# Kernel tuning notes

Measured on AMD Instinct MI355X. Metric: run time of the kernel, lower is better.

## Reference

```python
import jax, jax.numpy as jnp
import numpy as np
import math

B, N, E, H = 2, 4096, 256, 8
HS = E // H  # head_size = 32


def setup_inputs() -> dict:
    key = jax.random.key(0)
    ks = jax.random.split(key, 8)
    s = 1.0 / math.sqrt(E)
    return {
        "node_features": jax.random.normal(ks[0], (B, N, E), dtype=jnp.float32),
        "adj": jax.random.randint(ks[1], (B, N, N), 0, 2).astype(jnp.bool_),
        "Wq": jax.random.normal(ks[2], (E, E), dtype=jnp.float32) * s,
        "bq": jax.random.normal(ks[3], (E,), dtype=jnp.float32) * s,
        "Wk": jax.random.normal(ks[4], (E, E), dtype=jnp.float32) * s,
        "bk": jax.random.normal(ks[5], (E,), dtype=jnp.float32) * s,
        "Wv": jax.random.normal(ks[6], (E, E), dtype=jnp.float32) * s,
        "bv": jax.random.normal(ks[7], (E,), dtype=jnp.float32) * s,
    }


def _split_heads(x):
    # (B, N, E) -> (B, H, N, HS)
    return x.reshape(B, N, H, HS).transpose(0, 2, 1, 3)


def reference(node_features, adj, Wq, bq, Wk, bk, Wv, bv):
    # nn.Linear: x @ W.T + b
    Q = _split_heads(node_features @ Wq.T + bq)
    K = _split_heads(node_features @ Wk.T + bk)
    V = _split_heads(node_features @ Wv.T + bv)
    scores = jnp.einsum("bhnd,bhmd->bhnm", Q, K) / math.sqrt(HS)
    scores = jnp.where(adj[:, None, :, :], scores, -jnp.inf)
    probs = jax.nn.softmax(scores, axis=-1)
    out = jnp.einsum("bhnm,bhmd->bhnd", probs, V)
    # (B, H, N, HS) -> (B, N, E); note: original forward does NOT apply W_out
    return out.transpose(0, 2, 1, 3).reshape(B, N, E)
```

## Files before the change

### kernel.cpp

```cpp
#include <hip/hip_runtime.h>

typedef __attribute__((ext_vector_type(8))) short short8;
typedef __attribute__((ext_vector_type(4))) float f32x4;
typedef __attribute__((ext_vector_type(4))) unsigned short u16x4;

constexpr int cB = 2, cN = 4096, cE = 256, cH = 8, cHS = 32;

__device__ __forceinline__ unsigned short f2bf(float f) {
    unsigned int u = __builtin_bit_cast(unsigned int, f);
    u = (u + 0x7FFFu + ((u >> 16) & 1u)) >> 16;
    return (unsigned short)u;
}

__device__ __forceinline__ unsigned int cvt_pk_bf16(float lo, float hi) {
    unsigned int r;
    asm("v_cvt_pk_bf16_f32 %0, %1, %2" : "=v"(r) : "v"(lo), "v"(hi));
    return r;
}

__global__ __launch_bounds__(256) void cvt_x_kernel(const float* __restrict__ x,
                                                    unsigned short* __restrict__ xb) {
    int t = blockIdx.x * 256 + threadIdx.x;
    f32x4 v = *((const f32x4*)x + t);
    u16x4 o = { f2bf(v[0]), f2bf(v[1]), f2bf(v[2]), f2bf(v[3]) };
    *((u16x4*)xb + t) = o;
}

__global__ __launch_bounds__(256) void cvt_w_kernel(const float* __restrict__ Wq,
                                                    const float* __restrict__ Wk,
                                                    const float* __restrict__ Wv,
                                                    unsigned short* __restrict__ wcb) {
    int t = blockIdx.x * 256 + threadIdx.x;
    int f = t * 4;
    int o = f >> 8, i = f & 255;
    const float* src = (o < 256) ? Wq : (o < 512 ? Wk : Wv);
    f32x4 v = *(const f32x4*)(src + (size_t)(o & 255) * 256 + i);
    u16x4 ov = { f2bf(v[0]), f2bf(v[1]), f2bf(v[2]), f2bf(v[3]) };
    *((u16x4*)wcb + t) = ov;
}

__global__ __launch_bounds__(256) void bitpack_kernel(const int* __restrict__ adj,
                                                      unsigned long long* __restrict__ mask) {
    int lane = threadIdx.x & 63;
    int wave = blockIdx.x * 4 + (threadIdx.x >> 6);
    const int nwaves = 2048 * 4;
    const int nwords = cB * cN * cN / 64;
    for (int w = wave; w < nwords; w += nwaves) {
        int v = adj[(size_t)w * 64 + lane];
        unsigned long long bal = __ballot(v != 0);
        if (lane == 0) mask[w] = bal;
    }
}

__global__ __launch_bounds__(256) void qkv_proj_kernel(const unsigned short* __restrict__ xb,
                                                       const unsigned short* __restrict__ wcb,
                                                       const float* __restrict__ bq,
                                                       const float* __restrict__ bk,
                                                       const float* __restrict__ bv,
                                                       unsigned short* __restrict__ Qb,
                                                       unsigned short* __restrict__ Kb,
                                                       unsigned short* __restrict__ Vt) {
    const int wv = threadIdx.x >> 6, lane = threadIdx.x & 63;
    const int col = lane & 15, grp = lane >> 4;
    const int rowbase = blockIdx.x * 64 + wv * 16;
    const int colbase = blockIdx.y * 64;
    const float CE = 1.4426950408889634f * 0.17677669529663687f;
    f32x4 acc[4] = {};
    for (int kk = 0; kk < 8; ++kk) {
        short8 a = *(const short8*)(xb + (size_t)(rowbase + col) * 256 + kk * 32 + grp * 8);
        #pragma unroll
        for (int c = 0; c < 4; ++c) {
            short8 bf = *(const short8*)(wcb + (size_t)(colbase + c * 16 + col) * 256 + kk * 32 + grp * 8);
            acc[c] = __builtin_amdgcn_mfma_f32_16x16x32_bf16(a, bf, acc[c], 0, 0, 0);
        }
    }
    #pragma unroll
    for (int c = 0; c < 4; ++c) {
        const int o = colbase + c * 16 + col;
        const int sel = o >> 8, oo = o & 255;
        const float bias = (sel == 0 ? bq : sel == 1 ? bk : bv)[oo];
        const int h = oo >> 5, hs = oo & 31;
        const int R0 = rowbase + grp * 4;
        const int b = R0 >> 12, n0 = R0 & 4095;
        if (sel == 0) {
            #pragma unroll
            for (int r = 0; r < 4; ++r)
                Qb[(size_t)((b * cH + h) * cN + n0 + r) * cHS + hs] = f2bf((acc[c][r] + bias) * CE);
        } else if (sel == 1) {
            #pragma unroll
            for (int r = 0; r < 4; ++r)
                Kb[(size_t)((b * cH + h) * cN + n0 + r) * cHS + hs] = f2bf(acc[c][r] + bias);
        } else {
            unsigned short* vrow = Vt + (size_t)((b * cH + h) * cHS + hs) * cN;
            #pragma unroll
            for (int r = 0; r < 4; ++r) {
                const int n = n0 + r;
                const int pos = (n & ~31) + 2 * (n & 15) + ((n >> 4) & 1);
                vrow[pos] = f2bf(acc[c][r] + bias);
            }
        }
    }
}

__global__ __launch_bounds__(256, 4) void attn_kernel(const unsigned short* __restrict__ Qb,
                                                      const unsigned short* __restrict__ Kb,
                                                      const unsigned short* __restrict__ Vt,
                                                      const unsigned int* __restrict__ mask32,
                                                      float* __restrict__ out) {
    __shared__ float comb[4][64][24];
    const int wv = threadIdx.x >> 6, lane = threadIdx.x & 63;
    const int col = lane & 15, grp = lane >> 4;
    int bid = blockIdx.x;
    bid = (bid & 7) * 128 + (bid >> 3);
    const int qt0 = bid & 63, h = (bid >> 6) & 7, b = bid >> 9;
    const unsigned short* Qh = Qb + (size_t)(b * cH + h) * cN * cHS;
    const unsigned short* Kh = Kb + (size_t)(b * cH + h) * cN * cHS;
    const unsigned short* Vh = Vt + (size_t)(b * cH + h) * cHS * cN;
    unsigned int* pw = (unsigned int*)&comb[0][0][0] + wv * 640;
    const f32x4 z4 = {0.f, 0.f, 0.f, 0.f};
    const short8 ones = { 0x3F80, 0x3F80, 0x3F80, 0x3F80, 0x3F80, 0x3F80, 0x3F80, 0x3F80 };
    const int kt0 = wv * 32;

    #pragma unroll 1
    for (int tk = 0; tk < 2; ++tk) {
        const int qbase = (qt0 + tk * 64) * 32;
        const unsigned int* mrow = mask32 + (size_t)(b * cN + qbase) * 128;

        const short8 aq0 = *(const short8*)(Qh + (size_t)(qbase + col) * cHS + grp * 8);
        const short8 aq1 = *(const short8*)(Qh + (size_t)(qbase + 16 + col) * cHS + grp * 8);

        f32x4 acc[2][2] = {};
        f32x4 lacc[2] = {};

        short8 ck0 = *(const short8*)(Kh + (size_t)(kt0 * 32 + col) * cHS + grp * 8);
        short8 ck1 = *(const short8*)(Kh + (size_t)(kt0 * 32 + 16 + col) * cHS + grp * 8);
        short8 cv0 = *(const short8*)(Vh + (size_t)col * cN + kt0 * 32 + grp * 8);
        short8 cv1 = *(const short8*)(Vh + (size_t)(16 + col) * cN + kt0 * 32 + grp * 8);
        unsigned int cm[8];
        #pragma unroll
        for (int i = 0; i < 8; ++i)
            cm[i] = mrow[(size_t)((i >> 2) * 16 + grp * 4 + (i & 3)) * 128 + kt0];

        #pragma unroll 2
        for (int kt = kt0; kt < kt0 + 32; ++kt) {
            const short8 k0 = ck0, k1 = ck1, v0 = cv0, v1 = cv1;
            unsigned int m8[8];
            #pragma unroll
            for (int i = 0; i < 8; ++i) m8[i] = cm[i];
            if (kt < kt0 + 31) {
                const int kb = (kt + 1) * 32;
                ck0 = *(const short8*)(Kh + (size_t)(kb + col) * cHS + grp * 8);
                ck1 = *(const short8*)(Kh + (size_t)(kb + 16 + col) * cHS + grp * 8);
                cv0 = *(const short8*)(Vh + (size_t)col * cN + kb + grp * 8);
                cv1 = *(const short8*)(Vh + (size_t)(16 + col) * cN + kb + grp * 8);
                #pragma unroll
                for (int i = 0; i < 8; ++i)
                    cm[i] = mrow[(size_t)((i >> 2) * 16 + grp * 4 + (i & 3)) * 128 + kt + 1];
            }

            f32x4 s[2][2];
            s[0][0] = __builtin_amdgcn_mfma_f32_16x16x32_bf16(aq0, k0, z4, 0, 0, 0);
            s[0][1] = __builtin_amdgcn_mfma_f32_16x16x32_bf16(aq0, k1, z4, 0, 0, 0);
            s[1][0] = __builtin_amdgcn_mfma_f32_16x16x32_bf16(aq1, k0, z4, 0, 0, 0);
            s[1][1] = __builtin_amdgcn_mfma_f32_16x16x32_bf16(aq1, k1, z4, 0, 0, 0);

            #pragma unroll
            for (int qs = 0; qs < 2; ++qs) {
                #pragma unroll
                for (int r = 0; r < 4; ++r) {
                    const unsigned int w32 = m8[qs * 4 + r];
                    const float e0 = __builtin_exp2f(s[qs][0][r]);
                    const float e1 = __builtin_exp2f(s[qs][1][r]);
                    const unsigned int msk = ((w32 >> col) & 0x00010001u) * 0xFFFFu;
                    pw[qs * 320 + (grp * 4 + r) * 20 + col] = cvt_pk_bf16(e0, e1) & msk;
                }
            }
            #pragma unroll
            for (int qs = 0; qs < 2; ++qs) {
                const short8 pa = *(const short8*)(pw + qs * 320 + col * 20 + grp * 4);
                acc[qs][0] = __builtin_amdgcn_mfma_f32_16x16x32_bf16(pa, v0, acc[qs][0], 0, 0, 0);
                acc[qs][1] = __builtin_amdgcn_mfma_f32_16x16x32_bf16(pa, v1, acc[qs][1], 0, 0, 0);
                lacc[qs]   = __builtin_amdgcn_mfma_f32_16x16x32_bf16(pa, ones, lacc[qs], 0, 0, 0);
            }
        }

        __syncthreads();
        float* me = &comb[wv][lane][0];
        *(f32x4*)(me +  0) = acc[0][0];
        *(f32x4*)(me +  4) = acc[0][1];
        *(f32x4*)(me +  8) = acc[1][0];
        *(f32x4*)(me + 12) = acc[1][1];
        *(f32x4*)(me + 16) = lacc[0];
        *(f32x4*)(me + 20) = lacc[1];
        __syncthreads();

        const int sg = wv, qs2 = sg >> 1, half = sg & 1;
        f32x4 a = {0.f, 0.f, 0.f, 0.f};
        f32x4 l = {0.f, 0.f, 0.f, 0.f};
        #pragma unroll
        for (int w = 0; w < 4; ++w) {
            a += *(const f32x4*)&comb[w][lane][sg * 4];
            l += *(const f32x4*)&comb[w][lane][16 + qs2 * 4];
        }
        const int row0 = qbase + qs2 * 16 + grp * 4;
        #pragma unroll
        for (int j = 0; j < 4; ++j) {
            out[(size_t)(b * cN + row0 + j) * cE + h * 32 + half * 16 + col] = a[j] / l[j];
        }
        __syncthreads();
    }
}

extern "C" void kernel_launch(void* const* d_in, const int* in_sizes, int n_in,
                              void* d_out, int out_size, void* d_ws, size_t ws_size,
                              hipStream_t stream) {
    const float* x   = (const float*)d_in[0];
    const int*   adj = (const int*)d_in[1];
    const float* Wq  = (const float*)d_in[2];
    const float* bq  = (const float*)d_in[3];
    const float* Wk  = (const float*)d_in[4];
    const float* bk  = (const float*)d_in[5];
    const float* Wv  = (const float*)d_in[6];
    const float* bv  = (const float*)d_in[7];
    float* out = (float*)d_out;

    char* ws = (char*)d_ws;
    unsigned short* Xb  = (unsigned short*)(ws);
    unsigned short* Wcb = (unsigned short*)(ws + (4ull << 20));
    unsigned short* Qb  = (unsigned short*)(ws + (5ull << 20));
    unsigned short* Kb  = (unsigned short*)(ws + (9ull << 20));
    unsigned short* Vt  = (unsigned short*)(ws + (13ull << 20));
    unsigned long long* mask64 = (unsigned long long*)(ws + (17ull << 20));

    cvt_x_kernel<<<dim3(2048), dim3(256), 0, stream>>>(x, Xb);
    cvt_w_kernel<<<dim3(192), dim3(256), 0, stream>>>(Wq, Wk, Wv, Wcb);
    bitpack_kernel<<<dim3(2048), dim3(256), 0, stream>>>(adj, mask64);
    qkv_proj_kernel<<<dim3(128, 12), dim3(256), 0, stream>>>(Xb, Wcb, bq, bk, bv, Qb, Kb, Vt);
    attn_kernel<<<dim3(1024), dim3(256), 0, stream>>>(Qb, Kb, Vt, (const unsigned int*)mask64, out);
}
```

Before: 212.5 us.

## Software-pipeline attention loop: overlap PV MFMA of previous tile with current scores

Restructures the per-wave key loop into a skewed software pipeline. A prologue computes probabilities for the first tile, and each iteration then issues the P·V MFMAs for the previous tile before computing exp/mask/pack for the current tile. An epilogue drains the last tile. Mask words are now loaded in the same iteration they are used, while K is prefetched one tile ahead and V is loaded for the tile it is consumed in one iteration later. The goal is to hide MFMA latency behind exp work. The trade-offs are unroll 1 instead of 2 and less prefetch distance for the mask and V loads.

```diff
diff --git a/kernel.cpp b/kernel.cpp
--- a/kernel.cpp
+++ b/kernel.cpp
@@ -132,31 +132,42 @@
         f32x4 acc[2][2] = {};
         f32x4 lacc[2] = {};
 
-        short8 ck0 = *(const short8*)(Kh + (size_t)(kt0 * 32 + col) * cHS + grp * 8);
-        short8 ck1 = *(const short8*)(Kh + (size_t)(kt0 * 32 + 16 + col) * cHS + grp * 8);
-        short8 cv0 = *(const short8*)(Vh + (size_t)col * cN + kt0 * 32 + grp * 8);
-        short8 cv1 = *(const short8*)(Vh + (size_t)(16 + col) * cN + kt0 * 32 + grp * 8);
-        unsigned int cm[8];
-        #pragma unroll
-        for (int i = 0; i < 8; ++i)
-            cm[i] = mrow[(size_t)((i >> 2) * 16 + grp * 4 + (i & 3)) * 128 + kt0];
-
-        #pragma unroll 2
-        for (int kt = kt0; kt < kt0 + 32; ++kt) {
-            const short8 k0 = ck0, k1 = ck1, v0 = cv0, v1 = cv1;
+        short8 kc0 = *(const short8*)(Kh + (size_t)(kt0 * 32 + col) * cHS + grp * 8);
+        short8 kc1 = *(const short8*)(Kh + (size_t)(kt0 * 32 + 16 + col) * cHS + grp * 8);
+        short8 vp0 = *(const short8*)(Vh + (size_t)col * cN + kt0 * 32 + grp * 8);
+        short8 vp1 = *(const short8*)(Vh + (size_t)(16 + col) * cN + kt0 * 32 + grp * 8);
+        {
+            f32x4 s[2][2];
+            s[0][0] = __builtin_amdgcn_mfma_f32_16x16x32_bf16(aq0, kc0, z4, 0, 0, 0);
+            s[0][1] = __builtin_amdgcn_mfma_f32_16x16x32_bf16(aq0, kc1, z4, 0, 0, 0);
+            s[1][0] = __builtin_amdgcn_mfma_f32_16x16x32_bf16(aq1, kc0, z4, 0, 0, 0);
+            s[1][1] = __builtin_amdgcn_mfma_f32_16x16x32_bf16(aq1, kc1, z4, 0, 0, 0);
+            #pragma unroll
+            for (int qs = 0; qs < 2; ++qs)
+                #pragma unroll
+                for (int r = 0; r < 4; ++r) {
+                    const unsigned int w32 = mrow[(size_t)(qs * 16 + grp * 4 + r) * 128 + kt0];
+                    const float e0 = __builtin_exp2f(s[qs][0][r]);
+                    const float e1 = __builtin_exp2f(s[qs][1][r]);
+                    const unsigned int msk = ((w32 >> col) & 0x00010001u) * 0xFFFFu;
+                    pw[qs * 320 + (grp * 4 + r) * 20 + col] = cvt_pk_bf16(e0, e1) & msk;
+                }
+        }
+        short8 kn0 = *(const short8*)(Kh + (size_t)((kt0 + 1) * 32 + col) * cHS + grp * 8);
+        short8 kn1 = *(const short8*)(Kh + (size_t)((kt0 + 1) * 32 + 16 + col) * cHS + grp * 8);
+
+        #pragma unroll 1
+        for (int kt = kt0 + 1; kt < kt0 + 32; ++kt) {
+            const short8 k0 = kn0, k1 = kn1;
+            const int kb1 = (kt + 1) * 32;
+            kn0 = *(const short8*)(Kh + (size_t)(kb1 + col) * cHS + grp * 8);
+            kn1 = *(const short8*)(Kh + (size_t)(kb1 + 16 + col) * cHS + grp * 8);
+            const short8 vc0 = *(const short8*)(Vh + (size_t)col * cN + kt * 32 + grp * 8);
+            const short8 vc1 = *(const short8*)(Vh + (size_t)(16 + col) * cN + kt * 32 + grp * 8);
             unsigned int m8[8];
             #pragma unroll
-            for (int i = 0; i < 8; ++i) m8[i] = cm[i];
-            if (kt < kt0 + 31) {
-                const int kb = (kt + 1) * 32;
-                ck0 = *(const short8*)(Kh + (size_t)(kb + col) * cHS + grp * 8);
-                ck1 = *(const short8*)(Kh + (size_t)(kb + 16 + col) * cHS + grp * 8);
-                cv0 = *(const short8*)(Vh + (size_t)col * cN + kb + grp * 8);
-                cv1 = *(const short8*)(Vh + (size_t)(16 + col) * cN + kb + grp * 8);
-                #pragma unroll
-                for (int i = 0; i < 8; ++i)
-                    cm[i] = mrow[(size_t)((i >> 2) * 16 + grp * 4 + (i & 3)) * 128 + kt + 1];
-            }
+            for (int i = 0; i < 8; ++i)
+                m8[i] = mrow[(size_t)((i >> 2) * 16 + grp * 4 + (i & 3)) * 128 + kt];
 
             f32x4 s[2][2];
             s[0][0] = __builtin_amdgcn_mfma_f32_16x16x32_bf16(aq0, k0, z4, 0, 0, 0);
@@ -166,6 +177,14 @@
 
             #pragma unroll
             for (int qs = 0; qs < 2; ++qs) {
+                const short8 pa = *(const short8*)(pw + qs * 320 + col * 20 + grp * 4);
+                acc[qs][0] = __builtin_amdgcn_mfma_f32_16x16x32_bf16(pa, vp0, acc[qs][0], 0, 0, 0);
+                acc[qs][1] = __builtin_amdgcn_mfma_f32_16x16x32_bf16(pa, vp1, acc[qs][1], 0, 0, 0);
+                lacc[qs]   = __builtin_amdgcn_mfma_f32_16x16x32_bf16(pa, ones, lacc[qs], 0, 0, 0);
+            }
+
+            #pragma unroll
+            for (int qs = 0; qs < 2; ++qs)
                 #pragma unroll
                 for (int r = 0; r < 4; ++r) {
                     const unsigned int w32 = m8[qs * 4 + r];
@@ -174,14 +193,14 @@
                     const unsigned int msk = ((w32 >> col) & 0x00010001u) * 0xFFFFu;
                     pw[qs * 320 + (grp * 4 + r) * 20 + col] = cvt_pk_bf16(e0, e1) & msk;
                 }
-            }
-            #pragma unroll
-            for (int qs = 0; qs < 2; ++qs) {
-                const short8 pa = *(const short8*)(pw + qs * 320 + col * 20 + grp * 4);
-                acc[qs][0] = __builtin_amdgcn_mfma_f32_16x16x32_bf16(pa, v0, acc[qs][0], 0, 0, 0);
-                acc[qs][1] = __builtin_amdgcn_mfma_f32_16x16x32_bf16(pa, v1, acc[qs][1], 0, 0, 0);
-                lacc[qs]   = __builtin_amdgcn_mfma_f32_16x16x32_bf16(pa, ones, lacc[qs], 0, 0, 0);
-            }
+            vp0 = vc0; vp1 = vc1;
+        }
+        #pragma unroll
+        for (int qs = 0; qs < 2; ++qs) {
+            const short8 pa = *(const short8*)(pw + qs * 320 + col * 20 + grp * 4);
+            acc[qs][0] = __builtin_amdgcn_mfma_f32_16x16x32_bf16(pa, vp0, acc[qs][0], 0, 0, 0);
+            acc[qs][1] = __builtin_amdgcn_mfma_f32_16x16x32_bf16(pa, vp1, acc[qs][1], 0, 0, 0);
+            lacc[qs]   = __builtin_amdgcn_mfma_f32_16x16x32_bf16(pa, ones, lacc[qs], 0, 0, 0);
         }
 
         __syncthreads();
```

New measurement: 199.2 us. 6.2% less time.
